# Kernel optimization log

Measured on AMD Instinct MI355X. Metric: run time of the kernel, lower is better.

## Reference

```python
import jax, jax.numpy as jnp
import numpy as np

NUM_HEADS = 8
NUM_POINTS = 9


def _bilinear_sample(img, gx, gy):
    """grid_sample, mode=bilinear, padding=zeros, align_corners=True.
    img: (B, C, H, W); gx, gy: (B, M) pixel coords. Returns (B, C, M)."""
    Bc, C, H, W = img.shape
    imgf = img.reshape(Bc, C, H * W)
    x0 = jnp.floor(gx)
    y0 = jnp.floor(gy)
    wx1 = gx - x0
    wy1 = gy - y0

    def corner(xi, yi, w):
        valid = (xi >= 0) & (xi < W) & (yi >= 0) & (yi < H)
        xi_c = jnp.clip(xi, 0, W - 1).astype(jnp.int32)
        yi_c = jnp.clip(yi, 0, H - 1).astype(jnp.int32)
        idx = yi_c * W + xi_c  # (B, M)
        g = jax.vmap(lambda im, ix: im[:, ix])(imgf, idx)  # (B, C, M)
        return g * (w * valid)[:, None, :]

    return (corner(x0, y0, (1 - wx1) * (1 - wy1))
            + corner(x0 + 1, y0, wx1 * (1 - wy1))
            + corner(x0, y0 + 1, (1 - wx1) * wy1)
            + corner(x0 + 1, y0 + 1, wx1 * wy1))


def setup_inputs() -> dict:
    key = jax.random.key(0)
    ks = jax.random.split(key, 6)
    B, Hp, Wp, T, D = 4, 64, 64, 3, 256
    N = Hp * Wp
    Hh, P = NUM_HEADS, NUM_POINTS
    x = jax.random.normal(ks[0], (B, N, T, D), dtype=jnp.float32)
    # offset/attn projections: small random (orig inits them to 0, which is degenerate for testing)
    W_off = jax.random.normal(ks[1], (D, Hh * P * 2), dtype=jnp.float32) * 0.01
    b_off = jnp.zeros((Hh * P * 2,), dtype=jnp.float32)
    W_attn = jax.random.normal(ks[2], (D, Hh * P), dtype=jnp.float32) * 0.01
    b_attn = jnp.zeros((Hh * P,), dtype=jnp.float32)
    W_v = jax.random.normal(ks[3], (D, D), dtype=jnp.float32) * 0.02
    b_v = jnp.zeros((D,), dtype=jnp.float32)
    W_o = jax.random.normal(ks[4], (D, D), dtype=jnp.float32) * 0.02
    b_o = jnp.zeros((D,), dtype=jnp.float32)
    return {"x": x, "W_off": W_off, "b_off": b_off, "W_attn": W_attn,
            "b_attn": b_attn, "W_v": W_v, "b_v": b_v, "W_o": W_o,
            "b_o": b_o, "Hp": Hp, "Wp": Wp}


def reference(x, W_off, b_off, W_attn, b_attn, W_v, b_v, W_o, b_o, Hp, Wp):
    B, N, T, D = x.shape
    Hh, P = NUM_HEADS, NUM_POINTS
    dh = D // Hh

    query = x[:, :, T // 2]  # (B, N, D) middle frame
    offset = (query @ W_off + b_off).reshape(B, N, Hh, P, 2)
    attn = jax.nn.softmax((query @ W_attn + b_attn).reshape(B, N, Hh, P), axis=-1)

    # reference points in [-1, 1], xy order (x = width coord)
    gh, gw = jnp.meshgrid(jnp.arange(Hp, dtype=jnp.float32),
                          jnp.arange(Wp, dtype=jnp.float32), indexing='ij')
    ref = jnp.stack([gw, gh], axis=-1).reshape(N, 2)
    ref = ref / jnp.asarray([Wp - 1, Hp - 1], dtype=jnp.float32) * 2 - 1

    loc = ref[None, :, None, None, :] + offset  # (B, N, H, P, 2) normalized

    value = (x @ W_v + b_v).reshape(B, N, T, Hh, dh)
    # (B, H, T, dh, N) -> (B*H*T, dh, Hp, Wp)
    val = jnp.transpose(value, (0, 3, 2, 4, 1)).reshape(B * Hh * T, dh, Hp, Wp)

    # per-(b,h) grid, shared across frames; fold T into batch of the sampler
    grid = jnp.transpose(loc, (0, 2, 1, 3, 4))  # (B, H, N, P, 2)
    grid = jnp.broadcast_to(grid[:, :, None], (B, Hh, T, N, P, 2))
    grid = grid.reshape(B * Hh * T, N * P, 2)
    gx = (grid[..., 0] + 1) * 0.5 * (Wp - 1)
    gy = (grid[..., 1] + 1) * 0.5 * (Hp - 1)

    sampled = _bilinear_sample(val, gx, gy)  # (B*H*T, dh, N*P)
    sampled = sampled.reshape(B, Hh, T, dh, N, P)

    # weighted sum over points, summed over frames
    out = jnp.einsum('bhtdnp,bnhp->bnhd', sampled, attn).reshape(B, N, D)
    return out @ W_o + b_o
```

## Files before the change

### kernel.cpp

```cpp
#include <hip/hip_runtime.h>
#include <hip/hip_bf16.h>


#define NN_ 4096
#define DD_ 256
#define NH_ 8
#define NP_ 9
#define DH_ 32
#define MM_ 16384

typedef __attribute__((ext_vector_type(8))) short bf16x8;
typedef __attribute__((ext_vector_type(4))) short bf16x4;
typedef __attribute__((ext_vector_type(4))) float f32x4;

static __device__ __forceinline__ unsigned short f2bf(float f) {
  unsigned int u = __float_as_uint(f);
  u = (u + 0x7fff + ((u >> 16) & 1)) >> 16;
  return (unsigned short)u;
}
static __device__ __forceinline__ float bf2f(unsigned short h) {
  return __uint_as_float(((unsigned int)h) << 16);
}

__global__ __launch_bounds__(256) void prep_w(
    const float* __restrict__ W_off, const float* __restrict__ W_attn,
    const float* __restrict__ W_v, const float* __restrict__ W_o,
    const float* __restrict__ b_off, const float* __restrict__ b_attn,
    unsigned short* __restrict__ wvh, unsigned short* __restrict__ wvl,
    unsigned short* __restrict__ wch, unsigned short* __restrict__ wcl,
    unsigned short* __restrict__ woh, unsigned short* __restrict__ wol,
    float* __restrict__ bcat) {
  const int n = blockIdx.x, t = threadIdx.x;
  {
    float v = W_v[(size_t)t * 256 + n];
    unsigned short h = f2bf(v);
    wvh[n * 256 + t] = h; wvl[n * 256 + t] = f2bf(v - bf2f(h));
  }
  {
    float v = W_o[(size_t)t * 256 + n];
    unsigned short h = f2bf(v);
    woh[n * 256 + t] = h; wol[n * 256 + t] = f2bf(v - bf2f(h));
  }
  if (n < 216) {
    float v = (n < 144) ? W_off[(size_t)t * 144 + n] : W_attn[(size_t)t * 72 + (n - 144)];
    unsigned short h = f2bf(v);
    wch[n * 256 + t] = h; wcl[n * 256 + t] = f2bf(v - bf2f(h));
  }
  if (n == 0 && t < 216) bcat[t] = (t < 144) ? b_off[t] : b_attn[t - 144];
}

__global__ __launch_bounds__(256) void prep_a(const float* __restrict__ x,
                                              unsigned short* __restrict__ ash,
                                              unsigned short* __restrict__ asl) {
  const int gid = blockIdx.x * 256 + threadIdx.x;
  const int row = gid >> 6, c4 = (gid & 63) * 4;
  const float* xr = x + (size_t)row * 768 + c4;
  float4 a0 = *(const float4*)xr;
  float4 a1 = *(const float4*)(xr + 256);
  float4 a2 = *(const float4*)(xr + 512);
  float s[4] = {a0.x + a1.x + a2.x, a0.y + a1.y + a2.y,
                a0.z + a1.z + a2.z, a0.w + a1.w + a2.w};
  bf16x4 hv, lv;
#pragma unroll
  for (int j = 0; j < 4; ++j) {
    unsigned short h = f2bf(s[j]);
    hv[j] = (short)h;
    lv[j] = (short)f2bf(s[j] - bf2f(h));
  }
  *(bf16x4*)(ash + (size_t)row * 256 + c4) = hv;
  *(bf16x4*)(asl + (size_t)row * 256 + c4) = lv;
}

template <int MODE>
__global__ __launch_bounds__(256) void mgemm(const unsigned short* __restrict__ Ahi,
                                             const unsigned short* __restrict__ Alo,
                                             const float* __restrict__ X,
                                             const unsigned short* __restrict__ Bth,
                                             const unsigned short* __restrict__ Btl,
                                             const float* __restrict__ bias,
                                             float* __restrict__ Cout) {
  constexpr int NC = (MODE == 1) ? 216 : 256;
  __shared__ unsigned short Ah[128][64], Al[128][64], Bh[128][64], Bl[128][64];
  const int m0 = blockIdx.x * 128, n0 = blockIdx.y * 128;
  const int tid = threadIdx.x;
  const int wid = tid >> 6, lane = tid & 63;
  const int am = (wid >> 1) * 64, bn = (wid & 1) * 64;
  const int fr = lane & 15, kg = lane >> 4;

  f32x4 acc[4][4];
#pragma unroll
  for (int i = 0; i < 4; ++i)
#pragma unroll
    for (int j = 0; j < 4; ++j) acc[i][j] = (f32x4)(0.f);

  for (int k0 = 0; k0 < 256; k0 += 64) {
#pragma unroll
    for (int i = 0; i < 4; ++i) {
      int cid = i * 256 + tid;
      int r = cid >> 3, c = cid & 7;
      int dst = r * 64 + ((c ^ (r & 7)) * 8);
      bf16x8 hv, lv;
      if (MODE == 1) {
        const float* src = X + ((size_t)(m0 + r) * 3 + 1) * 256 + k0 + c * 8;
        float4 f0 = *(const float4*)src, f1 = *(const float4*)(src + 4);
        float vv[8] = {f0.x, f0.y, f0.z, f0.w, f1.x, f1.y, f1.z, f1.w};
#pragma unroll
        for (int j = 0; j < 8; ++j) {
          unsigned short h = f2bf(vv[j]);
          hv[j] = (short)h;
          lv[j] = (short)f2bf(vv[j] - bf2f(h));
        }
      } else {
        size_t off = (size_t)(m0 + r) * 256 + k0 + c * 8;
        hv = *(const bf16x8*)(Ahi + off);
        lv = *(const bf16x8*)(Alo + off);
      }
      *(bf16x8*)(&Ah[0][0] + dst) = hv;
      *(bf16x8*)(&Al[0][0] + dst) = lv;
    }
#pragma unroll
    for (int i = 0; i < 4; ++i) {
      int cid = i * 256 + tid;
      int r = cid >> 3, c = cid & 7;
      int dst = r * 64 + ((c ^ (r & 7)) * 8);
      bf16x8 hv = (bf16x8)(short)0, lv = (bf16x8)(short)0;
      int nrow = n0 + r;
      if (NC == 256 || nrow < NC) {
        size_t off = (size_t)nrow * 256 + k0 + c * 8;
        hv = *(const bf16x8*)(Bth + off);
        lv = *(const bf16x8*)(Btl + off);
      }
      *(bf16x8*)(&Bh[0][0] + dst) = hv;
      *(bf16x8*)(&Bl[0][0] + dst) = lv;
    }
    __syncthreads();

#pragma unroll
    for (int ks = 0; ks < 2; ++ks) {
      bf16x8 ah[4], al[4], bh[4], bl[4];
      const int kc = ks * 4 + kg;
#pragma unroll
      for (int mi = 0; mi < 4; ++mi) {
        int m = am + mi * 16 + fr;
        int o = m * 64 + ((kc ^ (m & 7)) * 8);
        ah[mi] = *(const bf16x8*)(&Ah[0][0] + o);
        al[mi] = *(const bf16x8*)(&Al[0][0] + o);
      }
#pragma unroll
      for (int ni = 0; ni < 4; ++ni) {
        int n = bn + ni * 16 + fr;
        int o = n * 64 + ((kc ^ (n & 7)) * 8);
        bh[ni] = *(const bf16x8*)(&Bh[0][0] + o);
        bl[ni] = *(const bf16x8*)(&Bl[0][0] + o);
      }
#pragma unroll
      for (int mi = 0; mi < 4; ++mi)
#pragma unroll
        for (int ni = 0; ni < 4; ++ni) {
          acc[mi][ni] = __builtin_amdgcn_mfma_f32_16x16x32_bf16(ah[mi], bh[ni], acc[mi][ni], 0, 0, 0);
          acc[mi][ni] = __builtin_amdgcn_mfma_f32_16x16x32_bf16(ah[mi], bl[ni], acc[mi][ni], 0, 0, 0);
          acc[mi][ni] = __builtin_amdgcn_mfma_f32_16x16x32_bf16(al[mi], bh[ni], acc[mi][ni], 0, 0, 0);
        }
    }
    __syncthreads();
  }

  const int ro = kg * 4;
#pragma unroll
  for (int mi = 0; mi < 4; ++mi)
#pragma unroll
    for (int ni = 0; ni < 4; ++ni) {
      int col = n0 + bn + ni * 16 + fr;
      if (MODE == 1 && col >= 216) continue;
      int rowb = m0 + am + mi * 16 + ro;
      float bv = bias[col] * (MODE == 0 ? 3.f : 1.f);
#pragma unroll
      for (int r = 0; r < 4; ++r) {
        int grow = rowb + r;
        float v = acc[mi][ni][r] + bv;
        if (MODE == 0) {
          int b = grow >> 12, nn = grow & 4095;
          int h = col >> 5, d = col & 31;
          Cout[(((size_t)(b * NH_ + h) << 12) + nn) * DH_ + d] = v;
        } else if (MODE == 1) {
          Cout[(size_t)grow * 216 + col] = v;
        } else {
          Cout[(size_t)grow * 256 + col] = v;
        }
      }
    }
}

__global__ __launch_bounds__(256) void sample_k(const float* __restrict__ valsum,
                                                const float* __restrict__ proj,
                                                unsigned short* __restrict__ ihi,
                                                unsigned short* __restrict__ ilo) {
  const int bid = blockIdx.x;
  const int row = ((bid & 7) << 11) + (bid >> 3);
  const int b = row >> 12, n = row & 4095;

  __shared__ int cidx[72][4];
  __shared__ float cw[72][4];
  __shared__ float sa[72];

  const int t = threadIdx.x;
  if (t < 72) {
    const float* pr = proj + (size_t)row * 216;
    float ox = pr[t * 2], oy = pr[t * 2 + 1];
    float gx = (float)(n & 63) + ox * 31.5f;
    float gy = (float)(n >> 6) + oy * 31.5f;
    float fx0 = floorf(gx), fy0 = floorf(gy);
    float wx1 = gx - fx0, wy1 = gy - fy0;
    float wx0 = 1.f - wx1, wy0 = 1.f - wy1;
    int x0 = (int)fx0, y0 = (int)fy0, x1 = x0 + 1, y1 = y0 + 1;
    bool vx0 = (x0 >= 0) & (x0 < 64), vx1 = (x1 >= 0) & (x1 < 64);
    bool vy0 = (y0 >= 0) & (y0 < 64), vy1 = (y1 >= 0) & (y1 < 64);
    int x0c = min(max(x0, 0), 63), x1c = min(max(x1, 0), 63);
    int y0c = min(max(y0, 0), 63), y1c = min(max(y1, 0), 63);
    cidx[t][0] = (y0c * 64 + x0c) * DH_; cw[t][0] = (vx0 & vy0) ? wx0 * wy0 : 0.f;
    cidx[t][1] = (y0c * 64 + x1c) * DH_; cw[t][1] = (vx1 & vy0) ? wx1 * wy0 : 0.f;
    cidx[t][2] = (y1c * 64 + x0c) * DH_; cw[t][2] = (vx0 & vy1) ? wx0 * wy1 : 0.f;
    cidx[t][3] = (y1c * 64 + x1c) * DH_; cw[t][3] = (vx1 & vy1) ? wx1 * wy1 : 0.f;
  }
  if (t < 8) {
    const float* pr = proj + (size_t)row * 216 + 144 + t * 9;
    float lg[9], mx = -1e30f;
#pragma unroll
    for (int p = 0; p < 9; ++p) { lg[p] = pr[p]; mx = fmaxf(mx, lg[p]); }
    float s = 0.f;
#pragma unroll
    for (int p = 0; p < 9; ++p) { lg[p] = __expf(lg[p] - mx); s += lg[p]; }
    float inv = 1.f / s;
#pragma unroll
    for (int p = 0; p < 9; ++p) sa[t * 9 + p] = lg[p] * inv;
  }
  __syncthreads();

  const int h = t >> 5, d = t & 31;
  const float* vb = valsum + (((size_t)(b * NH_ + h) << 12)) * DH_ + d;
  float acc = 0.f;
#pragma unroll
  for (int p = 0; p < 9; ++p) {
    const int hp = h * 9 + p;
    float s = 0.f;
#pragma unroll
    for (int k = 0; k < 4; ++k) s += cw[hp][k] * vb[cidx[hp][k]];
    acc += sa[hp] * s;
  }
  unsigned short hv = f2bf(acc);
  ihi[(size_t)row * 256 + t] = hv;
  ilo[(size_t)row * 256 + t] = f2bf(acc - bf2f(hv));
}

extern "C" void kernel_launch(void* const* d_in, const int* in_sizes, int n_in,
                              void* d_out, int out_size, void* d_ws, size_t ws_size,
                              hipStream_t stream) {
  const float* x      = (const float*)d_in[0];
  const float* W_off  = (const float*)d_in[1];
  const float* b_off  = (const float*)d_in[2];
  const float* W_attn = (const float*)d_in[3];
  const float* b_attn = (const float*)d_in[4];
  const float* W_v    = (const float*)d_in[5];
  const float* b_v    = (const float*)d_in[6];
  const float* W_o    = (const float*)d_in[7];
  const float* b_o    = (const float*)d_in[8];
  float* out = (float*)d_out;

  float* valsum = (float*)d_ws;
  float* proj   = valsum + (size_t)MM_ * 256;
  float* bcat   = proj + (size_t)MM_ * 216;
  unsigned short* ash = (unsigned short*)(bcat + 256);
  unsigned short* asl = ash + (size_t)MM_ * 256;
  unsigned short* wvh = asl + (size_t)MM_ * 256;
  unsigned short* wvl = wvh + 65536;
  unsigned short* wch = wvl + 65536;
  unsigned short* wcl = wch + 55296;
  unsigned short* woh = wcl + 55296;
  unsigned short* wol = woh + 65536;
  unsigned short* ihi = ash;
  unsigned short* ilo = asl;

  dim3 blk(256);
  prep_w<<<dim3(256), blk, 0, stream>>>(W_off, W_attn, W_v, W_o, b_off, b_attn,
                                        wvh, wvl, wch, wcl, woh, wol, bcat);
  prep_a<<<dim3(MM_ / 4), blk, 0, stream>>>(x, ash, asl);
  mgemm<0><<<dim3(128, 2), blk, 0, stream>>>(ash, asl, nullptr, wvh, wvl, b_v, valsum);
  mgemm<1><<<dim3(128, 2), blk, 0, stream>>>(nullptr, nullptr, x, wch, wcl, bcat, proj);
  sample_k<<<dim3(MM_), blk, 0, stream>>>(valsum, proj, ihi, ilo);
  mgemm<2><<<dim3(128, 2), blk, 0, stream>>>(ihi, ilo, nullptr, woh, wol, b_o, out);
}
```

Measured before the change: 191.7 us.

## Merge value/proj GEMMs, halve GEMM M-tile, vectorize sampler with 64-thread blocks

Fuses the value-projection and offset/attention GEMMs into one launch selected by blockIdx.y, and shrinks the GEMM M tile from 128 to 64 so each launch has more blocks to spread across CUs. The sampling kernel now uses 64 threads per row, each loading float4 channel vectors per corner, and writes bf16x4 hi/lo outputs. This cuts launch count, raises occupancy and widens gather loads, at the cost of less register reuse per GEMM tile and larger per-thread sampler work.

Measured after the change: 176.5 us. 1.09x faster.

```diff
diff --git a/kernel.cpp b/kernel.cpp
--- a/kernel.cpp
+++ b/kernel.cpp
@@ -2,10 +2,7 @@
 #include <hip/hip_bf16.h>
 
 
-#define NN_ 4096
-#define DD_ 256
 #define NH_ 8
-#define NP_ 9
 #define DH_ 32
 #define MM_ 16384
 
@@ -71,36 +68,38 @@
   *(bf16x4*)(asl + (size_t)row * 256 + c4) = lv;
 }
 
-template <int MODE>
-__global__ __launch_bounds__(256) void mgemm(const unsigned short* __restrict__ Ahi,
-                                             const unsigned short* __restrict__ Alo,
-                                             const float* __restrict__ X,
-                                             const unsigned short* __restrict__ Bth,
-                                             const unsigned short* __restrict__ Btl,
-                                             const float* __restrict__ bias,
-                                             float* __restrict__ Cout) {
-  constexpr int NC = (MODE == 1) ? 216 : 256;
-  __shared__ unsigned short Ah[128][64], Al[128][64], Bh[128][64], Bl[128][64];
-  const int m0 = blockIdx.x * 128, n0 = blockIdx.y * 128;
+__global__ __launch_bounds__(256) void mgemm01(
+    const unsigned short* __restrict__ Ahi, const unsigned short* __restrict__ Alo,
+    const float* __restrict__ X,
+    const unsigned short* __restrict__ Wvh, const unsigned short* __restrict__ Wvl,
+    const unsigned short* __restrict__ Wch, const unsigned short* __restrict__ Wcl,
+    const float* __restrict__ b_v, const float* __restrict__ bcat,
+    float* __restrict__ valsum, float* __restrict__ proj) {
+  __shared__ unsigned short Ah[64][64], Al[64][64], Bh[128][64], Bl[128][64];
+  const int mode1 = (blockIdx.y >= 2);
+  const int n0 = (blockIdx.y & 1) * 128;
+  const int m0 = blockIdx.x * 64;
   const int tid = threadIdx.x;
   const int wid = tid >> 6, lane = tid & 63;
-  const int am = (wid >> 1) * 64, bn = (wid & 1) * 64;
+  const int am = (wid >> 1) * 32, bn = (wid & 1) * 64;
   const int fr = lane & 15, kg = lane >> 4;
-
-  f32x4 acc[4][4];
-#pragma unroll
-  for (int i = 0; i < 4; ++i)
+  const unsigned short* Bth = mode1 ? Wch : Wvh;
+  const unsigned short* Btl = mode1 ? Wcl : Wvl;
+
+  f32x4 acc[2][4];
+#pragma unroll
+  for (int i = 0; i < 2; ++i)
 #pragma unroll
     for (int j = 0; j < 4; ++j) acc[i][j] = (f32x4)(0.f);
 
   for (int k0 = 0; k0 < 256; k0 += 64) {
 #pragma unroll
-    for (int i = 0; i < 4; ++i) {
+    for (int i = 0; i < 2; ++i) {
       int cid = i * 256 + tid;
       int r = cid >> 3, c = cid & 7;
       int dst = r * 64 + ((c ^ (r & 7)) * 8);
       bf16x8 hv, lv;
-      if (MODE == 1) {
+      if (mode1) {
         const float* src = X + ((size_t)(m0 + r) * 3 + 1) * 256 + k0 + c * 8;
         float4 f0 = *(const float4*)src, f1 = *(const float4*)(src + 4);
         float vv[8] = {f0.x, f0.y, f0.z, f0.w, f1.x, f1.y, f1.z, f1.w};
@@ -123,9 +122,9 @@
       int cid = i * 256 + tid;
       int r = cid >> 3, c = cid & 7;
       int dst = r * 64 + ((c ^ (r & 7)) * 8);
+      int nrow = n0 + r;
       bf16x8 hv = (bf16x8)(short)0, lv = (bf16x8)(short)0;
-      int nrow = n0 + r;
-      if (NC == 256 || nrow < NC) {
+      if (!mode1 || nrow < 216) {
         size_t off = (size_t)nrow * 256 + k0 + c * 8;
         hv = *(const bf16x8*)(Bth + off);
         lv = *(const bf16x8*)(Btl + off);
@@ -137,10 +136,10 @@
 
 #pragma unroll
     for (int ks = 0; ks < 2; ++ks) {
-      bf16x8 ah[4], al[4], bh[4], bl[4];
       const int kc = ks * 4 + kg;
-#pragma unroll
-      for (int mi = 0; mi < 4; ++mi) {
+      bf16x8 ah[2], al[2], bh[4], bl[4];
+#pragma unroll
+      for (int mi = 0; mi < 2; ++mi) {
         int m = am + mi * 16 + fr;
         int o = m * 64 + ((kc ^ (m & 7)) * 8);
         ah[mi] = *(const bf16x8*)(&Ah[0][0] + o);
@@ -154,7 +153,7 @@
         bl[ni] = *(const bf16x8*)(&Bl[0][0] + o);
       }
 #pragma unroll
-      for (int mi = 0; mi < 4; ++mi)
+      for (int mi = 0; mi < 2; ++mi)
 #pragma unroll
         for (int ni = 0; ni < 4; ++ni) {
           acc[mi][ni] = __builtin_amdgcn_mfma_f32_16x16x32_bf16(ah[mi], bh[ni], acc[mi][ni], 0, 0, 0);
@@ -167,34 +166,115 @@
 
   const int ro = kg * 4;
 #pragma unroll
-  for (int mi = 0; mi < 4; ++mi)
+  for (int mi = 0; mi < 2; ++mi)
 #pragma unroll
     for (int ni = 0; ni < 4; ++ni) {
       int col = n0 + bn + ni * 16 + fr;
-      if (MODE == 1 && col >= 216) continue;
+      if (mode1 && col >= 216) continue;
       int rowb = m0 + am + mi * 16 + ro;
-      float bv = bias[col] * (MODE == 0 ? 3.f : 1.f);
+      float bv = mode1 ? bcat[col] : b_v[col] * 3.f;
 #pragma unroll
       for (int r = 0; r < 4; ++r) {
         int grow = rowb + r;
         float v = acc[mi][ni][r] + bv;
-        if (MODE == 0) {
+        if (mode1) {
+          proj[(size_t)grow * 216 + col] = v;
+        } else {
           int b = grow >> 12, nn = grow & 4095;
           int h = col >> 5, d = col & 31;
-          Cout[(((size_t)(b * NH_ + h) << 12) + nn) * DH_ + d] = v;
-        } else if (MODE == 1) {
-          Cout[(size_t)grow * 216 + col] = v;
-        } else {
-          Cout[(size_t)grow * 256 + col] = v;
+          valsum[(((size_t)(b * NH_ + h) << 12) + nn) * DH_ + d] = v;
         }
       }
     }
 }
 
-__global__ __launch_bounds__(256) void sample_k(const float* __restrict__ valsum,
-                                                const float* __restrict__ proj,
-                                                unsigned short* __restrict__ ihi,
-                                                unsigned short* __restrict__ ilo) {
+__global__ __launch_bounds__(256) void mgemm2(
+    const unsigned short* __restrict__ Ahi, const unsigned short* __restrict__ Alo,
+    const unsigned short* __restrict__ Bth, const unsigned short* __restrict__ Btl,
+    const float* __restrict__ bias, float* __restrict__ Cout) {
+  __shared__ unsigned short Ah[64][64], Al[64][64], Bh[128][64], Bl[128][64];
+  const int n0 = blockIdx.y * 128;
+  const int m0 = blockIdx.x * 64;
+  const int tid = threadIdx.x;
+  const int wid = tid >> 6, lane = tid & 63;
+  const int am = (wid >> 1) * 32, bn = (wid & 1) * 64;
+  const int fr = lane & 15, kg = lane >> 4;
+
+  f32x4 acc[2][4];
+#pragma unroll
+  for (int i = 0; i < 2; ++i)
+#pragma unroll
+    for (int j = 0; j < 4; ++j) acc[i][j] = (f32x4)(0.f);
+
+  for (int k0 = 0; k0 < 256; k0 += 64) {
+#pragma unroll
+    for (int i = 0; i < 2; ++i) {
+      int cid = i * 256 + tid;
+      int r = cid >> 3, c = cid & 7;
+      int dst = r * 64 + ((c ^ (r & 7)) * 8);
+      size_t off = (size_t)(m0 + r) * 256 + k0 + c * 8;
+      *(bf16x8*)(&Ah[0][0] + dst) = *(const bf16x8*)(Ahi + off);
+      *(bf16x8*)(&Al[0][0] + dst) = *(const bf16x8*)(Alo + off);
+    }
+#pragma unroll
+    for (int i = 0; i < 4; ++i) {
+      int cid = i * 256 + tid;
+      int r = cid >> 3, c = cid & 7;
+      int dst = r * 64 + ((c ^ (r & 7)) * 8);
+      size_t off = (size_t)(n0 + r) * 256 + k0 + c * 8;
+      *(bf16x8*)(&Bh[0][0] + dst) = *(const bf16x8*)(Bth + off);
+      *(bf16x8*)(&Bl[0][0] + dst) = *(const bf16x8*)(Btl + off);
+    }
+    __syncthreads();
+
+#pragma unroll
+    for (int ks = 0; ks < 2; ++ks) {
+      const int kc = ks * 4 + kg;
+      bf16x8 ah[2], al[2], bh[4], bl[4];
+#pragma unroll
+      for (int mi = 0; mi < 2; ++mi) {
+        int m = am + mi * 16 + fr;
+        int o = m * 64 + ((kc ^ (m & 7)) * 8);
+        ah[mi] = *(const bf16x8*)(&Ah[0][0] + o);
+        al[mi] = *(const bf16x8*)(&Al[0][0] + o);
+      }
+#pragma unroll
+      for (int ni = 0; ni < 4; ++ni) {
+        int n = bn + ni * 16 + fr;
+        int o = n * 64 + ((kc ^ (n & 7)) * 8);
+        bh[ni] = *(const bf16x8*)(&Bh[0][0] + o);
+        bl[ni] = *(const bf16x8*)(&Bl[0][0] + o);
+      }
+#pragma unroll
+      for (int mi = 0; mi < 2; ++mi)
+#pragma unroll
+        for (int ni = 0; ni < 4; ++ni) {
+          acc[mi][ni] = __builtin_amdgcn_mfma_f32_16x16x32_bf16(ah[mi], bh[ni], acc[mi][ni], 0, 0, 0);
+          acc[mi][ni] = __builtin_amdgcn_mfma_f32_16x16x32_bf16(ah[mi], bl[ni], acc[mi][ni], 0, 0, 0);
+          acc[mi][ni] = __builtin_amdgcn_mfma_f32_16x16x32_bf16(al[mi], bh[ni], acc[mi][ni], 0, 0, 0);
+        }
+    }
+    __syncthreads();
+  }
+
+  const int ro = kg * 4;
+#pragma unroll
+  for (int mi = 0; mi < 2; ++mi)
+#pragma unroll
+    for (int ni = 0; ni < 4; ++ni) {
+      int col = n0 + bn + ni * 16 + fr;
+      int rowb = m0 + am + mi * 16 + ro;
+      float bv = bias[col];
+#pragma unroll
+      for (int r = 0; r < 4; ++r)
+        Cout[(size_t)(rowb + r) * 256 + col] = acc[mi][ni][r] + bv;
+    }
+}
+
+__global__ __launch_bounds__(64) void sample_k(const float* __restrict__ valsum,
+                                               const float* __restrict__ proj,
+                                               unsigned short* __restrict__ ihi,
+                                               unsigned short* __restrict__ ilo) {
   const int bid = blockIdx.x;
   const int row = ((bid & 7) << 11) + (bid >> 3);
   const int b = row >> 12, n = row & 4095;
@@ -204,9 +284,9 @@
   __shared__ float sa[72];
 
   const int t = threadIdx.x;
-  if (t < 72) {
-    const float* pr = proj + (size_t)row * 216;
-    float ox = pr[t * 2], oy = pr[t * 2 + 1];
+  const float* pr = proj + (size_t)row * 216;
+  for (int e = t; e < 72; e += 64) {
+    float ox = pr[e * 2], oy = pr[e * 2 + 1];
     float gx = (float)(n & 63) + ox * 31.5f;
     float gy = (float)(n >> 6) + oy * 31.5f;
     float fx0 = floorf(gx), fy0 = floorf(gy);
@@ -217,16 +297,16 @@
     bool vy0 = (y0 >= 0) & (y0 < 64), vy1 = (y1 >= 0) & (y1 < 64);
     int x0c = min(max(x0, 0), 63), x1c = min(max(x1, 0), 63);
     int y0c = min(max(y0, 0), 63), y1c = min(max(y1, 0), 63);
-    cidx[t][0] = (y0c * 64 + x0c) * DH_; cw[t][0] = (vx0 & vy0) ? wx0 * wy0 : 0.f;
-    cidx[t][1] = (y0c * 64 + x1c) * DH_; cw[t][1] = (vx1 & vy0) ? wx1 * wy0 : 0.f;
-    cidx[t][2] = (y1c * 64 + x0c) * DH_; cw[t][2] = (vx0 & vy1) ? wx0 * wy1 : 0.f;
-    cidx[t][3] = (y1c * 64 + x1c) * DH_; cw[t][3] = (vx1 & vy1) ? wx1 * wy1 : 0.f;
+    cidx[e][0] = (y0c * 64 + x0c) * DH_; cw[e][0] = (vx0 & vy0) ? wx0 * wy0 : 0.f;
+    cidx[e][1] = (y0c * 64 + x1c) * DH_; cw[e][1] = (vx1 & vy0) ? wx1 * wy0 : 0.f;
+    cidx[e][2] = (y1c * 64 + x0c) * DH_; cw[e][2] = (vx0 & vy1) ? wx0 * wy1 : 0.f;
+    cidx[e][3] = (y1c * 64 + x1c) * DH_; cw[e][3] = (vx1 & vy1) ? wx1 * wy1 : 0.f;
   }
   if (t < 8) {
-    const float* pr = proj + (size_t)row * 216 + 144 + t * 9;
+    const float* pa = pr + 144 + t * 9;
     float lg[9], mx = -1e30f;
 #pragma unroll
-    for (int p = 0; p < 9; ++p) { lg[p] = pr[p]; mx = fmaxf(mx, lg[p]); }
+    for (int p = 0; p < 9; ++p) { lg[p] = pa[p]; mx = fmaxf(mx, lg[p]); }
     float s = 0.f;
 #pragma unroll
     for (int p = 0; p < 9; ++p) { lg[p] = __expf(lg[p] - mx); s += lg[p]; }
@@ -236,20 +316,33 @@
   }
   __syncthreads();
 
-  const int h = t >> 5, d = t & 31;
-  const float* vb = valsum + (((size_t)(b * NH_ + h) << 12)) * DH_ + d;
-  float acc = 0.f;
+  const int h = t >> 3, d4 = (t & 7) * 4;
+  const float* vb = valsum + ((size_t)((b * NH_ + h) << 12)) * DH_ + d4;
+  float ax = 0.f, ay = 0.f, az = 0.f, aw = 0.f;
 #pragma unroll
   for (int p = 0; p < 9; ++p) {
     const int hp = h * 9 + p;
-    float s = 0.f;
-#pragma unroll
-    for (int k = 0; k < 4; ++k) s += cw[hp][k] * vb[cidx[hp][k]];
-    acc += sa[hp] * s;
-  }
-  unsigned short hv = f2bf(acc);
-  ihi[(size_t)row * 256 + t] = hv;
-  ilo[(size_t)row * 256 + t] = f2bf(acc - bf2f(hv));
+    float sx = 0.f, sy = 0.f, sz = 0.f, sw = 0.f;
+#pragma unroll
+    for (int c = 0; c < 4; ++c) {
+      float4 v = *(const float4*)(vb + cidx[hp][c]);
+      float w = cw[hp][c];
+      sx += w * v.x; sy += w * v.y; sz += w * v.z; sw += w * v.w;
+    }
+    float ap = sa[hp];
+    ax += ap * sx; ay += ap * sy; az += ap * sz; aw += ap * sw;
+  }
+  float av[4] = {ax, ay, az, aw};
+  bf16x4 hv, lv;
+#pragma unroll
+  for (int j = 0; j < 4; ++j) {
+    unsigned short hh = f2bf(av[j]);
+    hv[j] = (short)hh;
+    lv[j] = (short)f2bf(av[j] - bf2f(hh));
+  }
+  const size_t o = (size_t)row * 256 + t * 4;
+  *(bf16x4*)(ihi + o) = hv;
+  *(bf16x4*)(ilo + o) = lv;
 }
 
 extern "C" void kernel_launch(void* const* d_in, const int* in_sizes, int n_in,
@@ -280,12 +373,11 @@
   unsigned short* ihi = ash;
   unsigned short* ilo = asl;
 
-  dim3 blk(256);
-  prep_w<<<dim3(256), blk, 0, stream>>>(W_off, W_attn, W_v, W_o, b_off, b_attn,
-                                        wvh, wvl, wch, wcl, woh, wol, bcat);
-  prep_a<<<dim3(MM_ / 4), blk, 0, stream>>>(x, ash, asl);
-  mgemm<0><<<dim3(128, 2), blk, 0, stream>>>(ash, asl, nullptr, wvh, wvl, b_v, valsum);
-  mgemm<1><<<dim3(128, 2), blk, 0, stream>>>(nullptr, nullptr, x, wch, wcl, bcat, proj);
-  sample_k<<<dim3(MM_), blk, 0, stream>>>(valsum, proj, ihi, ilo);
-  mgemm<2><<<dim3(128, 2), blk, 0, stream>>>(ihi, ilo, nullptr, woh, wol, b_o, out);
-}
+  prep_w<<<dim3(256), dim3(256), 0, stream>>>(W_off, W_attn, W_v, W_o, b_off, b_attn,
+                                              wvh, wvl, wch, wcl, woh, wol, bcat);
+  prep_a<<<dim3(MM_ / 4), dim3(256), 0, stream>>>(x, ash, asl);
+  mgemm01<<<dim3(256, 4), dim3(256), 0, stream>>>(ash, asl, x, wvh, wvl, wch, wcl,
+                                                  b_v, bcat, valsum, proj);
+  sample_k<<<dim3(MM_), dim3(64), 0, stream>>>(valsum, proj, ihi, ilo);
+  mgemm2<<<dim3(256, 2), dim3(256), 0, stream>>>(ihi, ilo, woh, wol, b_o, out);
+}
```
